# Optimization experiments

Hardware: AMD Instinct MI355X
Metric: run time of the kernel (lower is better)

The kernel has to match this reference:

```python
import jax, jax.numpy as jnp
import numpy as np

H = 1024      # hidden_size
V = 50257     # output_size (vocab)
L = 512       # max_length


def setup_inputs() -> dict:
    key = jax.random.key(0)
    ks = jax.random.split(key, 12)
    s = 0.02
    return {
        "x": jax.random.randint(ks[0], (1,), 0, V),
        "encoder_outputs": jax.random.normal(ks[1], (L, H), jnp.float32),
        "hidden": jax.random.normal(ks[2], (1, 1, H), jnp.float32),
        # parameters
        "emb": jax.random.normal(ks[3], (V, H), jnp.float32) * s,
        "attn_W": jax.random.normal(ks[4], (L, 2 * H), jnp.float32) * s,
        "attn_b": jnp.zeros((L,), jnp.float32),
        "comb_W": jax.random.normal(ks[5], (H, 2 * H), jnp.float32) * s,
        "comb_b": jnp.zeros((H,), jnp.float32),
        "W_ih": jax.random.normal(ks[6], (3 * H, H), jnp.float32) * s,
        "W_hh": jax.random.normal(ks[7], (3 * H, H), jnp.float32) * s,
        "b_ih": jnp.zeros((3 * H,), jnp.float32),
        "b_hh": jnp.zeros((3 * H,), jnp.float32),
        "out_W": jax.random.normal(ks[8], (V, H), jnp.float32) * s,
        "out_b": jnp.zeros((V,), jnp.float32),
    }


def reference(x, encoder_outputs, hidden, emb, attn_W, attn_b, comb_W, comb_b,
              W_ih, W_hh, b_ih, b_hh, out_W, out_b):
    # embedded: [1, H]  (dropout_p=0 -> identity)
    embedded = emb[x]
    h0 = hidden[0]  # [1, H]
    # Bahdanau-style attention over encoder positions
    attn_weights = jax.nn.softmax(
        jnp.concatenate([embedded, h0], axis=1) @ attn_W.T + attn_b, axis=1)  # [1, L]
    attn_applied = attn_weights @ encoder_outputs  # [1, H]
    # combine + relu
    out = jnp.concatenate([embedded, attn_applied], axis=1) @ comb_W.T + comb_b
    out = jax.nn.relu(out)  # [1, H] -- GRU input
    # GRU cell (PyTorch gate ordering: r, z, n)
    gx = out @ W_ih.T + b_ih   # [1, 3H]
    gh = h0 @ W_hh.T + b_hh    # [1, 3H]
    gx_r, gx_z, gx_n = jnp.split(gx, 3, axis=1)
    gh_r, gh_z, gh_n = jnp.split(gh, 3, axis=1)
    r = jax.nn.sigmoid(gx_r + gh_r)
    z = jax.nn.sigmoid(gx_z + gh_z)
    n = jnp.tanh(gx_n + r * gh_n)
    h_new = (1.0 - z) * n + z * h0  # [1, H]
    # output projection + log_softmax
    logp = jax.nn.log_softmax(h_new @ out_W.T + out_b, axis=1)  # [1, V]
    return logp, attn_weights
```

## Files before the change

kernel.cpp:

```cpp
#include <hip/hip_runtime.h>
#include <math.h>

#define H 1024
#define V 50257
#define L 512
#define NPART ((V + 15) / 16)

__device__ inline float wave_reduce_sum(float v) {
    #pragma unroll
    for (int off = 32; off > 0; off >>= 1)
        v += __shfl_down(v, off, 64);
    return v;
}

__device__ inline float wave_reduce_max(float v) {
    #pragma unroll
    for (int off = 32; off > 0; off >>= 1)
        v = fmaxf(v, __shfl_down(v, off, 64));
    return v;
}

__device__ inline float dot4(float4 a, float4 b) {
    return a.x * b.x + a.y * b.y + a.z * b.z + a.w * b.w;
}

__global__ void scores_kernel(const int* __restrict__ x,
                              const float* __restrict__ emb,
                              const float* __restrict__ hidden,
                              const float* __restrict__ attn_W,
                              const float* __restrict__ attn_b,
                              float* __restrict__ scores) {
    const int l = blockIdx.x;
    const int t = threadIdx.x;
    const int xi = x[0];
    const float4* wrow = (const float4*)(attn_W + (size_t)l * (2 * H));
    const float4* ev = (const float4*)(emb + (size_t)xi * H);
    const float4* hv = (const float4*)hidden;
    float acc = dot4(ev[t], wrow[t]) + dot4(hv[t], wrow[t + 256]);
    __shared__ float sm[4];
    acc = wave_reduce_sum(acc);
    if ((t & 63) == 0) sm[t >> 6] = acc;
    __syncthreads();
    if (t == 0)
        scores[l] = sm[0] + sm[1] + sm[2] + sm[3] + attn_b[l];
}

__global__ void softmax512(const float* __restrict__ scores,
                           float* __restrict__ attnw,
                           float* __restrict__ out_attn,
                           float* __restrict__ attnap) {
    const int t = threadIdx.x;
    attnap[t] = 0.f;
    attnap[t + 512] = 0.f;
    __shared__ float sm[8];
    float v = scores[t];
    float m = wave_reduce_max(v);
    if ((t & 63) == 0) sm[t >> 6] = m;
    __syncthreads();
    float M = sm[0];
    #pragma unroll
    for (int i = 1; i < 8; ++i) M = fmaxf(M, sm[i]);
    float e = expf(v - M);
    __syncthreads();
    float s = wave_reduce_sum(e);
    if ((t & 63) == 0) sm[t >> 6] = s;
    __syncthreads();
    float S = 0.f;
    #pragma unroll
    for (int i = 0; i < 8; ++i) S += sm[i];
    float w = e / S;
    attnw[t] = w;
    out_attn[t] = w;
}

__global__ void attn_apply(const float* __restrict__ attnw,
                           const float* __restrict__ enc,
                           float* __restrict__ attnap) {
    const int h = blockIdx.x * 256 + threadIdx.x;
    const int l0 = blockIdx.y * 64;
    float acc = 0.f;
    #pragma unroll 8
    for (int i = 0; i < 64; ++i)
        acc += attnw[l0 + i] * enc[(size_t)(l0 + i) * H + h];
    atomicAdd(&attnap[h], acc);
}

__global__ void combine_relu(const int* __restrict__ x,
                             const float* __restrict__ emb,
                             const float* __restrict__ attnap,
                             const float* __restrict__ comb_W,
                             const float* __restrict__ comb_b,
                             float* __restrict__ gru_in) {
    const int r = blockIdx.x;
    const int t = threadIdx.x;
    const int xi = x[0];
    const float4* wrow = (const float4*)(comb_W + (size_t)r * (2 * H));
    const float4* ev = (const float4*)(emb + (size_t)xi * H);
    const float4* av = (const float4*)attnap;
    float acc = dot4(ev[t], wrow[t]) + dot4(av[t], wrow[t + 256]);
    __shared__ float sm[4];
    acc = wave_reduce_sum(acc);
    if ((t & 63) == 0) sm[t >> 6] = acc;
    __syncthreads();
    if (t == 0)
        gru_in[r] = fmaxf(sm[0] + sm[1] + sm[2] + sm[3] + comb_b[r], 0.f);
}

__global__ void gates_kernel(const float* __restrict__ W_ih,
                             const float* __restrict__ W_hh,
                             const float* __restrict__ b_ih,
                             const float* __restrict__ b_hh,
                             const float* __restrict__ gru_in,
                             const float* __restrict__ hidden,
                             float* __restrict__ gx,
                             float* __restrict__ gh) {
    const int b = blockIdx.x;
    const int t = threadIdx.x;
    const float* w;
    const float* vec;
    float bias;
    float* outp;
    int r;
    if (b < 3 * H) {
        r = b; w = W_ih + (size_t)r * H; vec = gru_in; bias = b_ih[r]; outp = gx;
    } else {
        r = b - 3 * H; w = W_hh + (size_t)r * H; vec = hidden; bias = b_hh[r]; outp = gh;
    }
    float acc = dot4(((const float4*)vec)[t], ((const float4*)w)[t]);
    __shared__ float sm[4];
    acc = wave_reduce_sum(acc);
    if ((t & 63) == 0) sm[t >> 6] = acc;
    __syncthreads();
    if (t == 0)
        outp[r] = sm[0] + sm[1] + sm[2] + sm[3] + bias;
}

__global__ void gru_cell(const float* __restrict__ gx,
                         const float* __restrict__ gh,
                         const float* __restrict__ hidden,
                         float* __restrict__ h_new) {
    const int i = blockIdx.x * blockDim.x + threadIdx.x;
    float r = 1.f / (1.f + expf(-(gx[i] + gh[i])));
    float z = 1.f / (1.f + expf(-(gx[H + i] + gh[H + i])));
    float n = tanhf(gx[2 * H + i] + r * gh[2 * H + i]);
    h_new[i] = (1.f - z) * n + z * hidden[i];
}

__global__ void logits_kernel(const float* __restrict__ out_W,
                              const float* __restrict__ out_b,
                              const float* __restrict__ h_new,
                              float* __restrict__ logits,
                              float* __restrict__ partials) {
    const int lid = threadIdx.x & 63;
    const int wid = threadIdx.x >> 6;
    __shared__ float sl[16];
    const float4* hv = (const float4*)h_new;
    float4 h0 = hv[lid], h1 = hv[64 + lid], h2 = hv[128 + lid], h3 = hv[192 + lid];
    const int vbase = blockIdx.x * 16 + wid * 4;
    #pragma unroll
    for (int rr = 0; rr < 4; ++rr) {
        const int v = vbase + rr;
        float val = -INFINITY;
        if (v < V) {
            const float4* wr = (const float4*)(out_W + (size_t)v * H);
            float acc = dot4(wr[lid], h0) + dot4(wr[64 + lid], h1)
                      + dot4(wr[128 + lid], h2) + dot4(wr[192 + lid], h3);
            acc = wave_reduce_sum(acc);
            if (lid == 0) { val = acc + out_b[v]; logits[v] = val; }
        }
        if (lid == 0) sl[wid * 4 + rr] = val;
    }
    __syncthreads();
    if (threadIdx.x == 0) {
        float M = -INFINITY;
        #pragma unroll
        for (int i = 0; i < 16; ++i) M = fmaxf(M, sl[i]);
        float S = 0.f;
        #pragma unroll
        for (int i = 0; i < 16; ++i) S += expf(sl[i] - M);
        partials[2 * blockIdx.x] = M;
        partials[2 * blockIdx.x + 1] = S;
    }
}

__global__ void finalize_kernel(float* __restrict__ logits,
                                const float* __restrict__ partials) {
    const int t = threadIdx.x;
    __shared__ float sm[8];
    float m = -INFINITY;
    for (int i = t; i < NPART; i += 512) m = fmaxf(m, partials[2 * i]);
    m = wave_reduce_max(m);
    if ((t & 63) == 0) sm[t >> 6] = m;
    __syncthreads();
    float M = sm[0];
    #pragma unroll
    for (int i = 1; i < 8; ++i) M = fmaxf(M, sm[i]);
    __syncthreads();
    float s = 0.f;
    for (int i = t; i < NPART; i += 512) s += partials[2 * i + 1] * expf(partials[2 * i] - M);
    s = wave_reduce_sum(s);
    if ((t & 63) == 0) sm[t >> 6] = s;
    __syncthreads();
    float S = 0.f;
    #pragma unroll
    for (int i = 0; i < 8; ++i) S += sm[i];
    const float red = M + logf(S);
    const int v = blockIdx.x * 512 + t;
    if (v < V) logits[v] -= red;
}

extern "C" void kernel_launch(void* const* d_in, const int* in_sizes, int n_in,
                              void* d_out, int out_size, void* d_ws, size_t ws_size,
                              hipStream_t stream) {
    const int*   x       = (const int*)d_in[0];
    const float* enc     = (const float*)d_in[1];
    const float* hidden  = (const float*)d_in[2];
    const float* emb     = (const float*)d_in[3];
    const float* attn_W  = (const float*)d_in[4];
    const float* attn_b  = (const float*)d_in[5];
    const float* comb_W  = (const float*)d_in[6];
    const float* comb_b  = (const float*)d_in[7];
    const float* W_ih    = (const float*)d_in[8];
    const float* W_hh    = (const float*)d_in[9];
    const float* b_ih    = (const float*)d_in[10];
    const float* b_hh    = (const float*)d_in[11];
    const float* out_W   = (const float*)d_in[12];
    const float* out_b   = (const float*)d_in[13];
    float* out = (float*)d_out;
    float* ws  = (float*)d_ws;

    float* scores   = ws;
    float* attnw    = ws + 512;
    float* attnap   = ws + 1024;
    float* gru_in   = ws + 2048;
    float* gx       = ws + 3072;
    float* gh       = ws + 6144;
    float* h_new    = ws + 9216;
    float* partials = ws + 10240;

    scores_kernel<<<L, 256, 0, stream>>>(x, emb, hidden, attn_W, attn_b, scores);
    softmax512<<<1, L, 0, stream>>>(scores, attnw, out + V, attnap);
    attn_apply<<<dim3(4, 8), 256, 0, stream>>>(attnw, enc, attnap);
    combine_relu<<<H, 256, 0, stream>>>(x, emb, attnap, comb_W, comb_b, gru_in);
    gates_kernel<<<6 * H, 256, 0, stream>>>(W_ih, W_hh, b_ih, b_hh, gru_in, hidden, gx, gh);
    gru_cell<<<H / 256, 256, 0, stream>>>(gx, gh, hidden, h_new);
    logits_kernel<<<NPART, 256, 0, stream>>>(out_W, out_b, h_new, out, partials);
    finalize_kernel<<<(V + 511) / 512, 512, 0, stream>>>(out, partials);
}
```

Measured before the change: 425.3 us.

## Fuse decoder step into six kernels with wave-per-row GEMVs

Merges the attention scores with the W_hh gate GEMV and the attnap zeroing into one launch. Fuses the softmax into attention-apply, recomputing the softmax redundantly in each block. Moves the GRU cell into the logits kernel, where each block recomputes h_new into shared memory. Switches the GEMVs to one wave per row, which drops the block-level shared-memory reduction and cuts launch count from eight to six. The cost is redundant softmax and GRU-cell arithmetic in every block of the fused kernels.

After: 419.9 us. Within noise of the previous version (-1.3%).

```diff
diff --git a/kernel.cpp b/kernel.cpp
--- a/kernel.cpp
+++ b/kernel.cpp
@@ -24,137 +24,180 @@
     return a.x * b.x + a.y * b.y + a.z * b.z + a.w * b.w;
 }
 
-__global__ void scores_kernel(const int* __restrict__ x,
-                              const float* __restrict__ emb,
-                              const float* __restrict__ hidden,
-                              const float* __restrict__ attn_W,
-                              const float* __restrict__ attn_b,
-                              float* __restrict__ scores) {
-    const int l = blockIdx.x;
-    const int t = threadIdx.x;
-    const int xi = x[0];
-    const float4* wrow = (const float4*)(attn_W + (size_t)l * (2 * H));
-    const float4* ev = (const float4*)(emb + (size_t)xi * H);
+__device__ inline float sigmoidf_(float x) { return 1.f / (1.f + expf(-x)); }
+
+__global__ void k1_scores_gh(const int* __restrict__ x,
+                             const float* __restrict__ emb,
+                             const float* __restrict__ hidden,
+                             const float* __restrict__ attn_W,
+                             const float* __restrict__ attn_b,
+                             const float* __restrict__ W_hh,
+                             const float* __restrict__ b_hh,
+                             float* __restrict__ scores,
+                             float* __restrict__ gh,
+                             float* __restrict__ attnap) {
+    const int b = blockIdx.x;
+    const int t = threadIdx.x;
+    const int lid = t & 63, wid = t >> 6;
     const float4* hv = (const float4*)hidden;
-    float acc = dot4(ev[t], wrow[t]) + dot4(hv[t], wrow[t + 256]);
-    __shared__ float sm[4];
-    acc = wave_reduce_sum(acc);
-    if ((t & 63) == 0) sm[t >> 6] = acc;
-    __syncthreads();
-    if (t == 0)
-        scores[l] = sm[0] + sm[1] + sm[2] + sm[3] + attn_b[l];
-}
-
-__global__ void softmax512(const float* __restrict__ scores,
-                           float* __restrict__ attnw,
-                           float* __restrict__ out_attn,
-                           float* __restrict__ attnap) {
-    const int t = threadIdx.x;
-    attnap[t] = 0.f;
-    attnap[t + 512] = 0.f;
-    __shared__ float sm[8];
-    float v = scores[t];
-    float m = wave_reduce_max(v);
-    if ((t & 63) == 0) sm[t >> 6] = m;
-    __syncthreads();
-    float M = sm[0];
-    #pragma unroll
-    for (int i = 1; i < 8; ++i) M = fmaxf(M, sm[i]);
-    float e = expf(v - M);
-    __syncthreads();
-    float s = wave_reduce_sum(e);
-    if ((t & 63) == 0) sm[t >> 6] = s;
-    __syncthreads();
-    float S = 0.f;
-    #pragma unroll
-    for (int i = 0; i < 8; ++i) S += sm[i];
-    float w = e / S;
-    attnw[t] = w;
-    out_attn[t] = w;
-}
-
-__global__ void attn_apply(const float* __restrict__ attnw,
-                           const float* __restrict__ enc,
-                           float* __restrict__ attnap) {
-    const int h = blockIdx.x * 256 + threadIdx.x;
-    const int l0 = blockIdx.y * 64;
+    if (b < 128) {
+        const int l = b * 4 + wid;
+        const int xi = x[0];
+        const float4* ev = (const float4*)(emb + (size_t)xi * H);
+        const float4* wrow = (const float4*)(attn_W + (size_t)l * (2 * H));
+        float acc = 0.f;
+        #pragma unroll
+        for (int k = 0; k < 4; ++k) {
+            int idx = k * 64 + lid;
+            acc += dot4(ev[idx], wrow[idx]);
+        }
+        #pragma unroll
+        for (int k = 0; k < 4; ++k) {
+            int idx = k * 64 + lid;
+            acc += dot4(hv[idx], wrow[256 + idx]);
+        }
+        acc = wave_reduce_sum(acc);
+        if (lid == 0) scores[l] = acc + attn_b[l];
+    } else if (b < 896) {
+        const int r = (b - 128) * 4 + wid;
+        const float4* wrow = (const float4*)(W_hh + (size_t)r * H);
+        float acc = 0.f;
+        #pragma unroll
+        for (int k = 0; k < 4; ++k) {
+            int idx = k * 64 + lid;
+            acc += dot4(hv[idx], wrow[idx]);
+        }
+        acc = wave_reduce_sum(acc);
+        if (lid == 0) gh[r] = acc + b_hh[r];
+    } else {
+        ((float4*)attnap)[t] = make_float4(0.f, 0.f, 0.f, 0.f);
+    }
+}
+
+__global__ void k2_softmax_apply(const float* __restrict__ scores,
+                                 const float* __restrict__ enc,
+                                 float* __restrict__ attnap,
+                                 float* __restrict__ out_attn) {
+    const int t = threadIdx.x;
+    __shared__ float smx[4], sms[4], sw[512];
+    float v0 = scores[t], v1 = scores[t + 256];
+    float m = wave_reduce_max(fmaxf(v0, v1));
+    if ((t & 63) == 0) smx[t >> 6] = m;
+    __syncthreads();
+    float M = fmaxf(fmaxf(smx[0], smx[1]), fmaxf(smx[2], smx[3]));
+    float e0 = expf(v0 - M), e1 = expf(v1 - M);
+    float s = wave_reduce_sum(e0 + e1);
+    if ((t & 63) == 0) sms[t >> 6] = s;
+    __syncthreads();
+    float S = sms[0] + sms[1] + sms[2] + sms[3];
+    float w0 = e0 / S, w1 = e1 / S;
+    sw[t] = w0;
+    sw[t + 256] = w1;
+    if (blockIdx.x == 0 && blockIdx.y == 0) {
+        out_attn[t] = w0;
+        out_attn[t + 256] = w1;
+    }
+    __syncthreads();
+    const int h = blockIdx.x * 256 + t;
+    const int l0 = blockIdx.y * 32;
     float acc = 0.f;
     #pragma unroll 8
-    for (int i = 0; i < 64; ++i)
-        acc += attnw[l0 + i] * enc[(size_t)(l0 + i) * H + h];
+    for (int i = 0; i < 32; ++i)
+        acc += sw[l0 + i] * enc[(size_t)(l0 + i) * H + h];
     atomicAdd(&attnap[h], acc);
 }
 
-__global__ void combine_relu(const int* __restrict__ x,
-                             const float* __restrict__ emb,
-                             const float* __restrict__ attnap,
-                             const float* __restrict__ comb_W,
-                             const float* __restrict__ comb_b,
-                             float* __restrict__ gru_in) {
-    const int r = blockIdx.x;
-    const int t = threadIdx.x;
+__global__ void k3_combine(const int* __restrict__ x,
+                           const float* __restrict__ emb,
+                           const float* __restrict__ attnap,
+                           const float* __restrict__ comb_W,
+                           const float* __restrict__ comb_b,
+                           float* __restrict__ gru_in) {
+    const int t = threadIdx.x;
+    const int lid = t & 63, wid = t >> 6;
+    const int r = blockIdx.x * 4 + wid;
     const int xi = x[0];
-    const float4* wrow = (const float4*)(comb_W + (size_t)r * (2 * H));
     const float4* ev = (const float4*)(emb + (size_t)xi * H);
     const float4* av = (const float4*)attnap;
-    float acc = dot4(ev[t], wrow[t]) + dot4(av[t], wrow[t + 256]);
-    __shared__ float sm[4];
+    const float4* wrow = (const float4*)(comb_W + (size_t)r * (2 * H));
+    float acc = 0.f;
+    #pragma unroll
+    for (int k = 0; k < 4; ++k) {
+        int idx = k * 64 + lid;
+        acc += dot4(ev[idx], wrow[idx]);
+    }
+    #pragma unroll
+    for (int k = 0; k < 4; ++k) {
+        int idx = k * 64 + lid;
+        acc += dot4(av[idx], wrow[256 + idx]);
+    }
     acc = wave_reduce_sum(acc);
-    if ((t & 63) == 0) sm[t >> 6] = acc;
-    __syncthreads();
-    if (t == 0)
-        gru_in[r] = fmaxf(sm[0] + sm[1] + sm[2] + sm[3] + comb_b[r], 0.f);
-}
-
-__global__ void gates_kernel(const float* __restrict__ W_ih,
-                             const float* __restrict__ W_hh,
-                             const float* __restrict__ b_ih,
-                             const float* __restrict__ b_hh,
-                             const float* __restrict__ gru_in,
-                             const float* __restrict__ hidden,
-                             float* __restrict__ gx,
-                             float* __restrict__ gh) {
-    const int b = blockIdx.x;
-    const int t = threadIdx.x;
-    const float* w;
-    const float* vec;
-    float bias;
-    float* outp;
-    int r;
-    if (b < 3 * H) {
-        r = b; w = W_ih + (size_t)r * H; vec = gru_in; bias = b_ih[r]; outp = gx;
-    } else {
-        r = b - 3 * H; w = W_hh + (size_t)r * H; vec = hidden; bias = b_hh[r]; outp = gh;
-    }
-    float acc = dot4(((const float4*)vec)[t], ((const float4*)w)[t]);
-    __shared__ float sm[4];
+    if (lid == 0) gru_in[r] = fmaxf(acc + comb_b[r], 0.f);
+}
+
+__global__ void k4_gx(const float* __restrict__ W_ih,
+                      const float* __restrict__ b_ih,
+                      const float* __restrict__ gru_in,
+                      float* __restrict__ gx) {
+    const int t = threadIdx.x;
+    const int lid = t & 63, wid = t >> 6;
+    const int r = blockIdx.x * 4 + wid;
+    const float4* vv = (const float4*)gru_in;
+    const float4* wrow = (const float4*)(W_ih + (size_t)r * H);
+    float acc = 0.f;
+    #pragma unroll
+    for (int k = 0; k < 4; ++k) {
+        int idx = k * 64 + lid;
+        acc += dot4(vv[idx], wrow[idx]);
+    }
     acc = wave_reduce_sum(acc);
-    if ((t & 63) == 0) sm[t >> 6] = acc;
-    __syncthreads();
-    if (t == 0)
-        outp[r] = sm[0] + sm[1] + sm[2] + sm[3] + bias;
-}
-
-__global__ void gru_cell(const float* __restrict__ gx,
-                         const float* __restrict__ gh,
-                         const float* __restrict__ hidden,
-                         float* __restrict__ h_new) {
-    const int i = blockIdx.x * blockDim.x + threadIdx.x;
-    float r = 1.f / (1.f + expf(-(gx[i] + gh[i])));
-    float z = 1.f / (1.f + expf(-(gx[H + i] + gh[H + i])));
-    float n = tanhf(gx[2 * H + i] + r * gh[2 * H + i]);
-    h_new[i] = (1.f - z) * n + z * hidden[i];
-}
-
-__global__ void logits_kernel(const float* __restrict__ out_W,
-                              const float* __restrict__ out_b,
-                              const float* __restrict__ h_new,
-                              float* __restrict__ logits,
-                              float* __restrict__ partials) {
-    const int lid = threadIdx.x & 63;
-    const int wid = threadIdx.x >> 6;
+    if (lid == 0) gx[r] = acc + b_ih[r];
+}
+
+__global__ void k5_cell_logits(const float* __restrict__ gx,
+                               const float* __restrict__ gh,
+                               const float* __restrict__ hidden,
+                               const float* __restrict__ out_W,
+                               const float* __restrict__ out_b,
+                               float* __restrict__ logits,
+                               float* __restrict__ partials) {
+    const int t = threadIdx.x;
+    __shared__ float sh[H];
     __shared__ float sl[16];
-    const float4* hv = (const float4*)h_new;
+    {
+        float4 xr = ((const float4*)gx)[t];
+        float4 xz = ((const float4*)(gx + H))[t];
+        float4 xn = ((const float4*)(gx + 2 * H))[t];
+        float4 hr = ((const float4*)gh)[t];
+        float4 hz = ((const float4*)(gh + H))[t];
+        float4 hn = ((const float4*)(gh + 2 * H))[t];
+        float4 h0 = ((const float4*)hidden)[t];
+        float4 o;
+        {
+            float r = sigmoidf_(xr.x + hr.x), z = sigmoidf_(xz.x + hz.x);
+            float n = tanhf(xn.x + r * hn.x);
+            o.x = (1.f - z) * n + z * h0.x;
+        }
+        {
+            float r = sigmoidf_(xr.y + hr.y), z = sigmoidf_(xz.y + hz.y);
+            float n = tanhf(xn.y + r * hn.y);
+            o.y = (1.f - z) * n + z * h0.y;
+        }
+        {
+            float r = sigmoidf_(xr.z + hr.z), z = sigmoidf_(xz.z + hz.z);
+            float n = tanhf(xn.z + r * hn.z);
+            o.z = (1.f - z) * n + z * h0.z;
+        }
+        {
+            float r = sigmoidf_(xr.w + hr.w), z = sigmoidf_(xz.w + hz.w);
+            float n = tanhf(xn.w + r * hn.w);
+            o.w = (1.f - z) * n + z * h0.w;
+        }
+        ((float4*)sh)[t] = o;
+    }
+    __syncthreads();
+    const int lid = t & 63, wid = t >> 6;
+    const float4* hv = (const float4*)sh;
     float4 h0 = hv[lid], h1 = hv[64 + lid], h2 = hv[128 + lid], h3 = hv[192 + lid];
     const int vbase = blockIdx.x * 16 + wid * 4;
     #pragma unroll
@@ -171,7 +214,7 @@
         if (lid == 0) sl[wid * 4 + rr] = val;
     }
     __syncthreads();
-    if (threadIdx.x == 0) {
+    if (t == 0) {
         float M = -INFINITY;
         #pragma unroll
         for (int i = 0; i < 16; ++i) M = fmaxf(M, sl[i]);
@@ -183,8 +226,8 @@
     }
 }
 
-__global__ void finalize_kernel(float* __restrict__ logits,
-                                const float* __restrict__ partials) {
+__global__ void k6_finalize(float* __restrict__ logits,
+                            const float* __restrict__ partials) {
     const int t = threadIdx.x;
     __shared__ float sm[8];
     float m = -INFINITY;
@@ -230,20 +273,17 @@
     float* ws  = (float*)d_ws;
 
     float* scores   = ws;
-    float* attnw    = ws + 512;
-    float* attnap   = ws + 1024;
-    float* gru_in   = ws + 2048;
-    float* gx       = ws + 3072;
-    float* gh       = ws + 6144;
-    float* h_new    = ws + 9216;
-    float* partials = ws + 10240;
-
-    scores_kernel<<<L, 256, 0, stream>>>(x, emb, hidden, attn_W, attn_b, scores);
-    softmax512<<<1, L, 0, stream>>>(scores, attnw, out + V, attnap);
-    attn_apply<<<dim3(4, 8), 256, 0, stream>>>(attnw, enc, attnap);
-    combine_relu<<<H, 256, 0, stream>>>(x, emb, attnap, comb_W, comb_b, gru_in);
-    gates_kernel<<<6 * H, 256, 0, stream>>>(W_ih, W_hh, b_ih, b_hh, gru_in, hidden, gx, gh);
-    gru_cell<<<H / 256, 256, 0, stream>>>(gx, gh, hidden, h_new);
-    logits_kernel<<<NPART, 256, 0, stream>>>(out_W, out_b, h_new, out, partials);
-    finalize_kernel<<<(V + 511) / 512, 512, 0, stream>>>(out, partials);
-}
+    float* attnap   = ws + 512;
+    float* gru_in   = ws + 1536;
+    float* gx       = ws + 2560;
+    float* gh       = ws + 5632;
+    float* partials = ws + 8704;
+
+    k1_scores_gh<<<897, 256, 0, stream>>>(x, emb, hidden, attn_W, attn_b,
+                                          W_hh, b_hh, scores, gh, attnap);
+    k2_softmax_apply<<<dim3(4, 16), 256, 0, stream>>>(scores, enc, attnap, out + V);
+    k3_combine<<<256, 256, 0, stream>>>(x, emb, attnap, comb_W, comb_b, gru_in);
+    k4_gx<<<768, 256, 0, stream>>>(W_ih, b_ih, gru_in, gx);
+    k5_cell_logits<<<NPART, 256, 0, stream>>>(gx, gh, hidden, out_W, out_b, out, partials);
+    k6_finalize<<<(V + 511) / 512, 512, 0, stream>>>(out, partials);
+}
```
